# Kernel tuning notes

Hardware: AMD Instinct MI355X
Metric: run time of the kernel (lower is better)

## Reference

```python
import jax, jax.numpy as jnp
import numpy as np
import math

D = 256        # embedding_size
NHEAD = 4
HD = D // NHEAD
FF = 2048      # torch TransformerEncoderLayer default dim_feedforward
NLAYER = 3
VOCAB = 30000
OLD = 2048     # resnet50 fc in_features
BPTT = 20
EOS = 2
PAD = 0
MAXLEN = 5000


def make_pe():
    position = np.arange(MAXLEN)[:, None].astype(np.float32)
    div_term = np.exp(np.arange(0, D, 2).astype(np.float32) * (-math.log(10000.0) / D))
    pe = np.zeros((MAXLEN, D), dtype=np.float32)
    pe[:, 0::2] = np.sin(position * div_term)
    pe[:, 1::2] = np.cos(position * div_term)
    return jnp.asarray(pe)  # [maxlen, d]

PE = make_pe()


def setup_inputs() -> dict:
    key = jax.random.key(0)
    ks = jax.random.split(key, 20)
    s = 0.02
    inp = {
        'image_feats': jax.random.normal(ks[0], (64, OLD), jnp.float32),
        'target_ingrs': jax.random.randint(ks[1], (64, BPTT), 0, VOCAB),
        'emb_table': jax.random.normal(ks[2], (VOCAB, D), jnp.float32) * s,
        'W_g2e': jax.random.normal(ks[3], (OLD, D), jnp.float32) * s,
        'b_g2e': jnp.zeros((D,), jnp.float32),
        'W_out': jax.random.normal(ks[4], (D, VOCAB), jnp.float32) * s,
        'b_out': jnp.zeros((VOCAB,), jnp.float32),
    }
    # per-layer transformer params
    Wqkv, bqkv, Wo, bo, W1, b1, W2, b2, g1, be1, g2, be2 = ([] for _ in range(12))
    k = ks[5]
    for l in range(NLAYER):
        k, *sub = jax.random.split(k, 7)
        Wqkv.append(jax.random.normal(sub[0], (D, 3 * D), jnp.float32) * s)
        bqkv.append(jnp.zeros((3 * D,), jnp.float32))
        Wo.append(jax.random.normal(sub[1], (D, D), jnp.float32) * s)
        bo.append(jnp.zeros((D,), jnp.float32))
        W1.append(jax.random.normal(sub[2], (D, FF), jnp.float32) * s)
        b1.append(jnp.zeros((FF,), jnp.float32))
        W2.append(jax.random.normal(sub[3], (FF, D), jnp.float32) * s)
        b2.append(jnp.zeros((D,), jnp.float32))
        g1.append(jnp.ones((D,), jnp.float32)); be1.append(jnp.zeros((D,), jnp.float32))
        g2.append(jnp.ones((D,), jnp.float32)); be2.append(jnp.zeros((D,), jnp.float32))
    stk = lambda xs: jnp.stack(xs)
    inp.update(Wqkv=stk(Wqkv), bqkv=stk(bqkv), Wo=stk(Wo), bo=stk(bo),
               W1=stk(W1), b1=stk(b1), W2=stk(W2), b2=stk(b2),
               g1=stk(g1), be1=stk(be1), g2=stk(g2), be2=stk(be2))
    return inp


def layernorm(x, g, b):
    mu = jnp.mean(x, -1, keepdims=True)
    var = jnp.var(x, -1, keepdims=True)
    return (x - mu) * jax.lax.rsqrt(var + 1e-5) * g + b


def encoder(x, params):
    # x: [S, B, D] (seq-first like torch). Post-norm encoder, ReLU FFN, no mask.
    (Wqkv, bqkv, Wo, bo, W1, b1, W2, b2, g1, be1, g2, be2) = params
    S, B, _ = x.shape
    for l in range(NLAYER):
        qkv = x @ Wqkv[l] + bqkv[l]                  # [S,B,3D]
        q, k, v = jnp.split(qkv, 3, axis=-1)
        def heads(t):  # [S,B,D] -> [B,H,S,hd]
            return t.reshape(S, B, NHEAD, HD).transpose(1, 2, 0, 3)
        q, k, v = heads(q), heads(k), heads(v)
        att = jnp.einsum('bhqd,bhkd->bhqk', q, k) / math.sqrt(HD)
        att = jax.nn.softmax(att, axis=-1)
        o = jnp.einsum('bhqk,bhkd->bhqd', att, v)    # [B,H,S,hd]
        o = o.transpose(2, 0, 1, 3).reshape(S, B, D)
        x = layernorm(x + o @ Wo[l] + bo[l], g1[l], be1[l])
        ff = jax.nn.relu(x @ W1[l] + b1[l]) @ W2[l] + b2[l]
        x = layernorm(x + ff, g2[l], be2[l])
    return x


def mask_from_eos_after(ids):
    # mult_before=False: mask[:,idx] = all(ids[:,1:idx+1] != EOS); mask[:,0]=1
    ne = (ids != EOS)
    ne = ne.at[:, 0].set(True)
    return jnp.cumprod(ne.astype(jnp.int32), axis=1)  # [B,S]


def reference(image_feats, target_ingrs, emb_table, W_g2e, b_g2e, W_out, b_out,
              Wqkv, bqkv, Wo, bo, W1, b1, W2, b2, g1, be1, g2, be2):
    params = (Wqkv, bqkv, Wo, bo, W1, b1, W2, b2, g1, be1, g2, be2)
    B = image_feats.shape[0]
    img_embed = image_feats @ W_g2e + b_g2e          # [B,D]
    bptt = target_ingrs.shape[1]

    # embeds buffer: [bptt, B, D]; position 0 = image embed (note: original code
    # never applies pos_encoder in predict(), so neither do we)
    embeds = jnp.zeros((bptt, B, D), jnp.float32).at[0].set(img_embed)

    probs_steps = []
    words_steps = []
    # loop over decode steps (fixed-length Python loop; each step re-encodes prefix,
    # faithful to original no-KV-cache behavior)
    for i in range(bptt):
        seq = embeds[: i + 1]                        # [i+1, B, D]
        out = encoder(seq, params)[-1]               # [B, D]
        logits = out @ W_out + b_out                 # [B, V]
        sm = jax.nn.softmax(logits, axis=-1)
        widx = jnp.argmax(sm, axis=-1)               # [B]
        probs_steps.append(sm)
        words_steps.append(widx)
        if i + 1 < bptt:
            embeds = embeds.at[i + 1].set(emb_table[widx])

    decoder_out = jnp.stack(probs_steps, axis=1)     # [B, bptt, V]
    sampled_word = jnp.stack(words_steps, axis=1)    # [B, bptt]
    eos = decoder_out[:, :, EOS]
    mask = mask_from_eos_after(target_ingrs)         # [B, bptt] int
    ingr_probs = jnp.max(decoder_out * mask[:, :, None].astype(jnp.float32), axis=1)
    sampled_word = jnp.where(mask == 0, PAD, sampled_word)
    return ingr_probs, sampled_word, eos
```

## Files before the change

kernel.cpp:

```cpp
#include <hip/hip_runtime.h>
#include <math.h>

#define D 256
#define NH 4
#define HDIM 64
#define FFD 2048
#define NL 3
#define VOC 30000
#define BPTT 20
#define BATCH 64
#define NMAX (BPTT*BATCH)

__global__ void k_mask(const int* __restrict__ ids, int* __restrict__ mask) {
  int b = threadIdx.x;
  int run = 1;
  for (int j = 0; j < BPTT; ++j) {
    if (j > 0 && ids[b*BPTT + j] == 2) run = 0;
    mask[b*BPTT + j] = run;
  }
}

__global__ __launch_bounds__(256) void k_img(const float* __restrict__ feats,
                                             const float* __restrict__ Wg,
                                             const float* __restrict__ bg,
                                             float* __restrict__ embeds) {
  __shared__ float xs[2048];
  int b = blockIdx.x, tid = threadIdx.x;
  for (int j = 0; j < 8; ++j) xs[tid + j*256] = feats[b*2048 + tid + j*256];
  __syncthreads();
  float acc = 0.f;
  for (int k = 0; k < 2048; k += 4) {
    float4 xv = *(const float4*)&xs[k];
    acc += xv.x * Wg[(k+0)*D + tid];
    acc += xv.y * Wg[(k+1)*D + tid];
    acc += xv.z * Wg[(k+2)*D + tid];
    acc += xv.w * Wg[(k+3)*D + tid];
  }
  embeds[b*D + tid] = acc + bg[tid];
}

__global__ __launch_bounds__(256) void k_gemm8(
    const float* __restrict__ A, int lda,
    const float* __restrict__ W,
    const float* __restrict__ bias,
    float* __restrict__ C, long pstride,
    int klen, int M, int relu)
{
  __shared__ float As[8][256];
  const int tid  = threadIdx.x;
  const int tok0 = blockIdx.x * 8;
  const int colb = blockIdx.y * 256;
  const int z    = blockIdx.z;
  const int kbeg = z * klen;
  C += (long)z * pstride;
  const int colg = tid & 63;
  const int tokg = tid >> 6;
  const int col  = colb + colg*4;
  int colL = col;
  if (colL > M-4) colL = M-4;

  float acc[2][4] = {{0.f,0.f,0.f,0.f},{0.f,0.f,0.f,0.f}};

  for (int k0 = 0; k0 < klen; k0 += 256) {
    __syncthreads();
#pragma unroll
    for (int j = 0; j < 8; ++j)
      As[j][tid] = A[(long)(tok0 + j)*lda + kbeg + k0 + tid];
    __syncthreads();
    const float* Wp = W + (long)(kbeg + k0)*M + colL;
#pragma unroll 2
    for (int kk = 0; kk < 256; kk += 4) {
      float a[2][4], w[4][4];
      *(float4*)a[0] = *(const float4*)&As[tokg*2+0][kk];
      *(float4*)a[1] = *(const float4*)&As[tokg*2+1][kk];
      *(float4*)w[0] = *(const float4*)(Wp + (long)(kk+0)*M);
      *(float4*)w[1] = *(const float4*)(Wp + (long)(kk+1)*M);
      *(float4*)w[2] = *(const float4*)(Wp + (long)(kk+2)*M);
      *(float4*)w[3] = *(const float4*)(Wp + (long)(kk+3)*M);
#pragma unroll
      for (int j = 0; j < 2; ++j)
#pragma unroll
        for (int c = 0; c < 4; ++c)
#pragma unroll
          for (int q = 0; q < 4; ++q)
            acc[j][c] += a[j][q] * w[q][c];
    }
  }

  if (col < M) {
    float bv[4] = {0.f,0.f,0.f,0.f};
    if (bias) *(float4*)bv = *(const float4*)(bias + col);
#pragma unroll
    for (int j = 0; j < 2; ++j) {
      float v[4];
#pragma unroll
      for (int c = 0; c < 4; ++c) {
        v[c] = acc[j][c] + bv[c];
        if (relu) v[c] = fmaxf(v[c], 0.f);
      }
      *(float4*)(C + (long)(tok0 + tokg*2 + j)*M + col) = *(float4*)v;
    }
  }
}

__global__ __launch_bounds__(256) void k_resln(
    const float* __restrict__ x, const float* __restrict__ parts, int nparts, long pstride,
    const float* __restrict__ bias, const float* __restrict__ g, const float* __restrict__ be,
    float* __restrict__ out)
{
  __shared__ float red[4];
  int tok = blockIdx.x, tid = threadIdx.x;
  float v = x[(long)tok*D + tid] + bias[tid];
  for (int p = 0; p < nparts; ++p) v += parts[(long)p*pstride + (long)tok*D + tid];

  float s = v;
  for (int off = 32; off; off >>= 1) s += __shfl_down(s, off);
  if ((tid & 63) == 0) red[tid >> 6] = s;
  __syncthreads();
  float mu = (red[0]+red[1]+red[2]+red[3]) * (1.0f/D);
  __syncthreads();
  float dv = v - mu;
  float q = dv*dv;
  for (int off = 32; off; off >>= 1) q += __shfl_down(q, off);
  if ((tid & 63) == 0) red[tid >> 6] = q;
  __syncthreads();
  float var = (red[0]+red[1]+red[2]+red[3]) * (1.0f/D);
  float inv = 1.0f / sqrtf(var + 1e-5f);
  out[(long)tok*D + tid] = dv * inv * g[tid] + be[tid];
}

__global__ __launch_bounds__(64) void k_attn(const float* __restrict__ qkv,
                                             float* __restrict__ o, int S)
{
  __shared__ float qs[BPTT*HDIM], ks[BPTT*HDIM], vs[BPTT*HDIM], ps[BPTT*(BPTT+1)];
  int bh = blockIdx.x;
  int b = bh & 63, h = bh >> 6;
  int d = threadIdx.x;
  for (int s = 0; s < S; ++s) {
    long base = (long)(s*BATCH + b)*(3*D) + h*HDIM + d;
    qs[s*HDIM+d] = qkv[base];
    ks[s*HDIM+d] = qkv[base + D];
    vs[s*HDIM+d] = qkv[base + 2*D];
  }
  __syncthreads();
  for (int p = d; p < S*S; p += 64) {
    int si = p / S, ti = p - si*S;
    float acc = 0.f;
#pragma unroll 4
    for (int k = 0; k < HDIM; ++k) acc += qs[si*HDIM+k] * ks[ti*HDIM+k];
    ps[si*(BPTT+1)+ti] = acc * 0.125f;
  }
  __syncthreads();
  if (d < S) {
    float m = -1e30f;
    for (int t = 0; t < S; ++t) m = fmaxf(m, ps[d*(BPTT+1)+t]);
    float sum = 0.f;
    for (int t = 0; t < S; ++t) { float e = expf(ps[d*(BPTT+1)+t] - m); ps[d*(BPTT+1)+t] = e; sum += e; }
    float inv = 1.0f / sum;
    for (int t = 0; t < S; ++t) ps[d*(BPTT+1)+t] *= inv;
  }
  __syncthreads();
  for (int s = 0; s < S; ++s) {
    float acc = 0.f;
    for (int t = 0; t < S; ++t) acc += ps[s*(BPTT+1)+t] * vs[t*HDIM+d];
    o[(long)(s*BATCH+b)*D + h*HDIM + d] = acc;
  }
}

__global__ __launch_bounds__(256) void k_vocab(
    const float* __restrict__ logits, const int* __restrict__ mask,
    float* __restrict__ out_probs, float* __restrict__ out_words, float* __restrict__ out_eos,
    const float* __restrict__ emb, float* __restrict__ embeds, int step)
{
  __shared__ float redA[4];
  __shared__ float r_s[4];
  __shared__ float r_em[4];
  __shared__ int   r_ei[4];
  int b = blockIdx.x, tid = threadIdx.x;
  const float* lrow = logits + (long)b*VOC;

  float m = -1e30f;
  for (int c = tid; c < VOC; c += 256) m = fmaxf(m, lrow[c]);
  for (int off = 32; off; off >>= 1) m = fmaxf(m, __shfl_down(m, off));
  if ((tid & 63) == 0) redA[tid >> 6] = m;
  __syncthreads();
  float gmax = fmaxf(fmaxf(redA[0],redA[1]), fmaxf(redA[2],redA[3]));
  __syncthreads();

  float s = 0.f, em = -1.0f;
  int ei = VOC;
  for (int c = tid; c < VOC; c += 256) {
    float e = expf(lrow[c] - gmax);
    s += e;
    if (e > em) { em = e; ei = c; }
  }
  for (int off = 32; off; off >>= 1) {
    float em2 = __shfl_down(em, off);
    int   ei2 = __shfl_down(ei, off);
    if (em2 > em || (em2 == em && ei2 < ei)) { em = em2; ei = ei2; }
    s += __shfl_down(s, off);
  }
  if ((tid & 63) == 0) { r_s[tid>>6] = s; r_em[tid>>6] = em; r_ei[tid>>6] = ei; }
  __syncthreads();
  float Ssum = r_s[0]+r_s[1]+r_s[2]+r_s[3];
  em = r_em[0]; ei = r_ei[0];
  for (int w = 1; w < 4; ++w)
    if (r_em[w] > em || (r_em[w] == em && r_ei[w] < ei)) { em = r_em[w]; ei = r_ei[w]; }

  int mk = mask[b*BPTT + step];

  for (int c = tid; c < VOC; c += 256) {
    float p = expf(lrow[c] - gmax) / Ssum;
    float* op = out_probs + (long)b*VOC + c;
    if (step == 0) *op = p;
    else if (mk)   *op = fmaxf(*op, p);
    if (c == 2) out_eos[b*BPTT + step] = p;
  }
  if (tid == 0) out_words[b*BPTT + step] = mk ? (float)ei : 0.0f;
  if (step + 1 < BPTT)
    embeds[(long)((step+1)*BATCH + b)*D + tid] = emb[(long)ei*D + tid];
}

extern "C" void kernel_launch(void* const* d_in, const int* in_sizes, int n_in,
                              void* d_out, int out_size, void* d_ws, size_t ws_size,
                              hipStream_t stream) {
  const float* image_feats = (const float*)d_in[0];
  const int*   target      = (const int*)  d_in[1];
  const float* emb_table   = (const float*)d_in[2];
  const float* W_g2e       = (const float*)d_in[3];
  const float* b_g2e       = (const float*)d_in[4];
  const float* W_out       = (const float*)d_in[5];
  const float* b_out       = (const float*)d_in[6];
  const float* Wqkv        = (const float*)d_in[7];
  const float* bqkv        = (const float*)d_in[8];
  const float* Wo          = (const float*)d_in[9];
  const float* bo          = (const float*)d_in[10];
  const float* W1          = (const float*)d_in[11];
  const float* b1          = (const float*)d_in[12];
  const float* W2          = (const float*)d_in[13];
  const float* b2          = (const float*)d_in[14];
  const float* g1          = (const float*)d_in[15];
  const float* be1         = (const float*)d_in[16];
  const float* g2          = (const float*)d_in[17];
  const float* be2         = (const float*)d_in[18];

  float* out_probs = (float*)d_out;
  float* out_words = out_probs + (long)BATCH*VOC;
  float* out_eos   = out_words + BATCH*BPTT;

  char* ws = (char*)d_ws;
  float* embeds = (float*)ws;  ws += sizeof(float)*(long)NMAX*D;
  float* xbuf   = (float*)ws;  ws += sizeof(float)*(long)NMAX*D;
  float* qkvb   = (float*)ws;  ws += sizeof(float)*(long)NMAX*3*D;
  float* obuf   = (float*)ws;  ws += sizeof(float)*(long)NMAX*D;
  float* pbuf   = (float*)ws;  ws += sizeof(float)*(long)4*NMAX*D;
  float* ffb    = (float*)ws;  ws += sizeof(float)*(long)NMAX*FFD;
  float* logits = (float*)ws;  ws += sizeof(float)*(long)BATCH*VOC;
  int*   maskb  = (int*)ws;    ws += sizeof(int)*BATCH*BPTT;

  k_mask<<<1, 64, 0, stream>>>(target, maskb);
  k_img<<<64, 256, 0, stream>>>(image_feats, W_g2e, b_g2e, embeds);

  for (int i = 0; i < BPTT; ++i) {
    int N = (i+1)*BATCH;
    for (int l = 0; l < NL; ++l) {
      const float* X = (l == 0) ? embeds : xbuf;
      k_gemm8<<<dim3(N/8, 3, 1), 256, 0, stream>>>(X, D, Wqkv + (long)l*D*3*D, bqkv + (long)l*3*D,
                                                   qkvb, 0, D, 3*D, 0);
      k_attn<<<dim3(BATCH*NH), 64, 0, stream>>>(qkvb, obuf, i+1);
      k_gemm8<<<dim3(N/8, 1, 1), 256, 0, stream>>>(obuf, D, Wo + (long)l*D*D, nullptr,
                                                   pbuf, 0, D, D, 0);
      k_resln<<<dim3(N), 256, 0, stream>>>(X, pbuf, 1, 0, bo + (long)l*D, g1 + (long)l*D, be1 + (long)l*D, xbuf);
      k_gemm8<<<dim3(N/8, FFD/256, 1), 256, 0, stream>>>(xbuf, D, W1 + (long)l*D*FFD, b1 + (long)l*FFD,
                                                         ffb, 0, D, FFD, 1);
      k_gemm8<<<dim3(N/8, 1, 4), 256, 0, stream>>>(ffb, FFD, W2 + (long)l*FFD*D, nullptr,
                                                   pbuf, (long)NMAX*D, FFD/4, D, 0);
      k_resln<<<dim3(N), 256, 0, stream>>>(xbuf, pbuf, 4, (long)NMAX*D, b2 + (long)l*D, g2 + (long)l*D, be2 + (long)l*D, xbuf);
    }
    k_gemm8<<<dim3(BATCH/8, (VOC+255)/256, 1), 256, 0, stream>>>(xbuf + (long)i*BATCH*D, D, W_out, b_out,
                                                                 logits, 0, D, VOC, 0);
    k_vocab<<<dim3(BATCH), 256, 0, stream>>>(logits, maskb, out_probs, out_words, out_eos,
                                             emb_table, embeds, i);
  }
}
```

Before: 10.89 ms.

## Retile GEMM to 32x128 blocks and fuse out-projection with residual LayerNorm

Replaces the 8-token GEMM kernel with a 32-token by 128-column tiled kernel that stages A in small padded shared-memory chunks. Each weight load is now reused across four tokens per thread instead of two. Adds a fused kernel that does the attention output projection, bias, residual add and LayerNorm in one pass, removing a separate kernel launch and an intermediate buffer round trip. Larger token tiles give fewer blocks for small early steps, and the vocab GEMM now has only 2 row blocks.

```diff
diff --git a/kernel.cpp b/kernel.cpp
--- a/kernel.cpp
+++ b/kernel.cpp
@@ -39,46 +39,53 @@
   embeds[b*D + tid] = acc + bg[tid];
 }
 
-__global__ __launch_bounds__(256) void k_gemm8(
+__global__ __launch_bounds__(256) void k_gemm32(
     const float* __restrict__ A, int lda,
     const float* __restrict__ W,
     const float* __restrict__ bias,
     float* __restrict__ C, long pstride,
     int klen, int M, int relu)
 {
-  __shared__ float As[8][256];
+  __shared__ float As[32][36];
   const int tid  = threadIdx.x;
-  const int tok0 = blockIdx.x * 8;
-  const int colb = blockIdx.y * 256;
+  const int tok0 = blockIdx.x * 32;
+  const int colb = blockIdx.y * 128;
   const int z    = blockIdx.z;
   const int kbeg = z * klen;
   C += (long)z * pstride;
-  const int colg = tid & 63;
-  const int tokg = tid >> 6;
+
+  const int colg = tid & 31;
+  const int tokg = tid >> 5;
   const int col  = colb + colg*4;
-  int colL = col;
-  if (colL > M-4) colL = M-4;
-
-  float acc[2][4] = {{0.f,0.f,0.f,0.f},{0.f,0.f,0.f,0.f}};
-
-  for (int k0 = 0; k0 < klen; k0 += 256) {
+  int colL = col; if (colL > M-4) colL = M-4;
+
+  const int sr = tid >> 3;
+  const int sc = (tid & 7) * 4;
+
+  float acc[4][4];
+#pragma unroll
+  for (int j = 0; j < 4; ++j)
+#pragma unroll
+    for (int c = 0; c < 4; ++c) acc[j][c] = 0.f;
+
+  for (int k0 = 0; k0 < klen; k0 += 32) {
     __syncthreads();
-#pragma unroll
-    for (int j = 0; j < 8; ++j)
-      As[j][tid] = A[(long)(tok0 + j)*lda + kbeg + k0 + tid];
+    *(float4*)&As[sr][sc] = *(const float4*)&A[(long)(tok0 + sr)*lda + kbeg + k0 + sc];
     __syncthreads();
     const float* Wp = W + (long)(kbeg + k0)*M + colL;
-#pragma unroll 2
-    for (int kk = 0; kk < 256; kk += 4) {
-      float a[2][4], w[4][4];
-      *(float4*)a[0] = *(const float4*)&As[tokg*2+0][kk];
-      *(float4*)a[1] = *(const float4*)&As[tokg*2+1][kk];
+#pragma unroll
+    for (int kk = 0; kk < 32; kk += 4) {
+      float w[4][4], a[4][4];
       *(float4*)w[0] = *(const float4*)(Wp + (long)(kk+0)*M);
       *(float4*)w[1] = *(const float4*)(Wp + (long)(kk+1)*M);
       *(float4*)w[2] = *(const float4*)(Wp + (long)(kk+2)*M);
       *(float4*)w[3] = *(const float4*)(Wp + (long)(kk+3)*M);
-#pragma unroll
-      for (int j = 0; j < 2; ++j)
+      *(float4*)a[0] = *(const float4*)&As[tokg*4+0][kk];
+      *(float4*)a[1] = *(const float4*)&As[tokg*4+1][kk];
+      *(float4*)a[2] = *(const float4*)&As[tokg*4+2][kk];
+      *(float4*)a[3] = *(const float4*)&As[tokg*4+3][kk];
+#pragma unroll
+      for (int j = 0; j < 4; ++j)
 #pragma unroll
         for (int c = 0; c < 4; ++c)
 #pragma unroll
@@ -91,15 +98,97 @@
     float bv[4] = {0.f,0.f,0.f,0.f};
     if (bias) *(float4*)bv = *(const float4*)(bias + col);
 #pragma unroll
-    for (int j = 0; j < 2; ++j) {
+    for (int j = 0; j < 4; ++j) {
       float v[4];
 #pragma unroll
       for (int c = 0; c < 4; ++c) {
         v[c] = acc[j][c] + bv[c];
         if (relu) v[c] = fmaxf(v[c], 0.f);
       }
-      *(float4*)(C + (long)(tok0 + tokg*2 + j)*M + col) = *(float4*)v;
+      *(float4*)(C + (long)(tok0 + tokg*4 + j)*M + col) = *(float4*)v;
     }
+  }
+}
+
+__global__ __launch_bounds__(256) void k_projln(
+    const float* __restrict__ Aop,
+    const float* __restrict__ W,
+    const float* __restrict__ X,
+    const float* __restrict__ bias,
+    const float* __restrict__ g, const float* __restrict__ be,
+    float* __restrict__ out)
+{
+  __shared__ float As[16][68];
+  const int tid  = threadIdx.x;
+  const int tok0 = blockIdx.x * 16;
+  const int colg = tid & 63;
+  const int tokg = tid >> 6;
+  const int col  = colg * 4;
+
+  const int sr = tid >> 4;
+  const int sc = (tid & 15) * 4;
+
+  float acc[4][4];
+#pragma unroll
+  for (int j = 0; j < 4; ++j)
+#pragma unroll
+    for (int c = 0; c < 4; ++c) acc[j][c] = 0.f;
+
+  for (int k0 = 0; k0 < 256; k0 += 64) {
+    __syncthreads();
+    *(float4*)&As[sr][sc] = *(const float4*)&Aop[(long)(tok0 + sr)*D + k0 + sc];
+    __syncthreads();
+    const float* Wp = W + (long)k0*D + col;
+#pragma unroll
+    for (int kk = 0; kk < 64; kk += 4) {
+      float w[4][4], a[4][4];
+      *(float4*)w[0] = *(const float4*)(Wp + (long)(kk+0)*D);
+      *(float4*)w[1] = *(const float4*)(Wp + (long)(kk+1)*D);
+      *(float4*)w[2] = *(const float4*)(Wp + (long)(kk+2)*D);
+      *(float4*)w[3] = *(const float4*)(Wp + (long)(kk+3)*D);
+      *(float4*)a[0] = *(const float4*)&As[tokg*4+0][kk];
+      *(float4*)a[1] = *(const float4*)&As[tokg*4+1][kk];
+      *(float4*)a[2] = *(const float4*)&As[tokg*4+2][kk];
+      *(float4*)a[3] = *(const float4*)&As[tokg*4+3][kk];
+#pragma unroll
+      for (int j = 0; j < 4; ++j)
+#pragma unroll
+        for (int c = 0; c < 4; ++c)
+#pragma unroll
+          for (int q = 0; q < 4; ++q)
+            acc[j][c] += a[j][q] * w[q][c];
+    }
+  }
+
+  float bv[4], gv[4], bev[4];
+  *(float4*)bv  = *(const float4*)(bias + col);
+  *(float4*)gv  = *(const float4*)(g + col);
+  *(float4*)bev = *(const float4*)(be + col);
+
+#pragma unroll
+  for (int j = 0; j < 4; ++j) {
+    const int tok = tok0 + tokg*4 + j;
+    float v[4];
+    float4 xv = *(const float4*)(X + (long)tok*D + col);
+    v[0] = acc[j][0] + bv[0] + xv.x;
+    v[1] = acc[j][1] + bv[1] + xv.y;
+    v[2] = acc[j][2] + bv[2] + xv.z;
+    v[3] = acc[j][3] + bv[3] + xv.w;
+    float s = v[0]+v[1]+v[2]+v[3];
+#pragma unroll
+    for (int off = 1; off < 64; off <<= 1) s += __shfl_xor(s, off);
+    float mu = s * (1.0f/D);
+    float q0=v[0]-mu, q1=v[1]-mu, q2=v[2]-mu, q3=v[3]-mu;
+    float q = q0*q0+q1*q1+q2*q2+q3*q3;
+#pragma unroll
+    for (int off = 1; off < 64; off <<= 1) q += __shfl_xor(q, off);
+    float inv = 1.0f / sqrtf(q * (1.0f/D) + 1e-5f);
+    float o[4];
+    o[0] = q0*inv*gv[0] + bev[0];
+    o[1] = q1*inv*gv[1] + bev[1];
+    o[2] = q2*inv*gv[2] + bev[2];
+    o[3] = q3*inv*gv[3] + bev[3];
+    *(float4*)(out + (long)tok*D + col) = *(float4*)o;
   }
 }
 
@@ -265,20 +354,19 @@
     int N = (i+1)*BATCH;
     for (int l = 0; l < NL; ++l) {
       const float* X = (l == 0) ? embeds : xbuf;
-      k_gemm8<<<dim3(N/8, 3, 1), 256, 0, stream>>>(X, D, Wqkv + (long)l*D*3*D, bqkv + (long)l*3*D,
-                                                   qkvb, 0, D, 3*D, 0);
+      k_gemm32<<<dim3(N/32, 6, 1), 256, 0, stream>>>(X, D, Wqkv + (long)l*D*3*D, bqkv + (long)l*3*D,
+                                                     qkvb, 0, D, 3*D, 0);
       k_attn<<<dim3(BATCH*NH), 64, 0, stream>>>(qkvb, obuf, i+1);
-      k_gemm8<<<dim3(N/8, 1, 1), 256, 0, stream>>>(obuf, D, Wo + (long)l*D*D, nullptr,
-                                                   pbuf, 0, D, D, 0);
-      k_resln<<<dim3(N), 256, 0, stream>>>(X, pbuf, 1, 0, bo + (long)l*D, g1 + (long)l*D, be1 + (long)l*D, xbuf);
-      k_gemm8<<<dim3(N/8, FFD/256, 1), 256, 0, stream>>>(xbuf, D, W1 + (long)l*D*FFD, b1 + (long)l*FFD,
-                                                         ffb, 0, D, FFD, 1);
-      k_gemm8<<<dim3(N/8, 1, 4), 256, 0, stream>>>(ffb, FFD, W2 + (long)l*FFD*D, nullptr,
-                                                   pbuf, (long)NMAX*D, FFD/4, D, 0);
+      k_projln<<<dim3(N/16), 256, 0, stream>>>(obuf, Wo + (long)l*D*D, X, bo + (long)l*D,
+                                               g1 + (long)l*D, be1 + (long)l*D, xbuf);
+      k_gemm32<<<dim3(N/32, FFD/128, 1), 256, 0, stream>>>(xbuf, D, W1 + (long)l*D*FFD, b1 + (long)l*FFD,
+                                                           ffb, 0, D, FFD, 1);
+      k_gemm32<<<dim3(N/32, 2, 4), 256, 0, stream>>>(ffb, FFD, W2 + (long)l*FFD*D, nullptr,
+                                                     pbuf, (long)NMAX*D, FFD/4, D, 0);
       k_resln<<<dim3(N), 256, 0, stream>>>(xbuf, pbuf, 4, (long)NMAX*D, b2 + (long)l*D, g2 + (long)l*D, be2 + (long)l*D, xbuf);
     }
-    k_gemm8<<<dim3(BATCH/8, (VOC+255)/256, 1), 256, 0, stream>>>(xbuf + (long)i*BATCH*D, D, W_out, b_out,
-                                                                 logits, 0, D, VOC, 0);
+    k_gemm32<<<dim3(BATCH/32, (VOC+127)/128, 1), 256, 0, stream>>>(xbuf + (long)i*BATCH*D, D, W_out, b_out,
+                                                                   logits, 0, D, VOC, 0);
     k_vocab<<<dim3(BATCH), 256, 0, stream>>>(logits, maskb, out_probs, out_words, out_eos,
                                              emb_table, embeds, i);
   }
```

Result: slower. 18.37 ms (+68.7%).

## Replace per-stage launches with one persistent cooperative megakernel using grid syncs

Applied to the files above, without the earlier changes.

Replaces the roughly 400 small kernel launches with a single cooperative persistent kernel. Each stage is a grid-stride loop over tiles, separated by grid.sync. The out-projection GEMM is fused with residual-add and LayerNorm, and attention now uses 256 threads per unit with a padded K buffer. This aims to remove launch overhead and idle gaps between the many tiny dependent kernels, at the cost of grid-wide barriers and a fixed grid size (at most 512 blocks). A multi-launch fallback runs if the cooperative launch fails.

```diff
diff --git a/kernel.cpp b/kernel.cpp
--- a/kernel.cpp
+++ b/kernel.cpp
@@ -1,5 +1,8 @@
 #include <hip/hip_runtime.h>
+#include <hip/hip_cooperative_groups.h>
 #include <math.h>
+
+namespace cg = cooperative_groups;
 
 #define D 256
 #define NH 4
@@ -11,21 +14,264 @@
 #define BATCH 64
 #define NMAX (BPTT*BATCH)
 
-__global__ void k_mask(const int* __restrict__ ids, int* __restrict__ mask) {
-  int b = threadIdx.x;
-  int run = 1;
-  for (int j = 0; j < BPTT; ++j) {
-    if (j > 0 && ids[b*BPTT + j] == 2) run = 0;
-    mask[b*BPTT + j] = run;
-  }
-}
-
-__global__ __launch_bounds__(256) void k_img(const float* __restrict__ feats,
-                                             const float* __restrict__ Wg,
-                                             const float* __restrict__ bg,
-                                             float* __restrict__ embeds) {
-  __shared__ float xs[2048];
-  int b = blockIdx.x, tid = threadIdx.x;
+struct Args {
+  const float* image_feats; const int* target; const float* emb_table;
+  const float* W_g2e; const float* b_g2e; const float* W_out; const float* b_out;
+  const float* Wqkv; const float* bqkv; const float* Wo; const float* bo;
+  const float* W1; const float* b1; const float* W2; const float* b2;
+  const float* g1; const float* be1; const float* g2; const float* be2;
+  float* out_probs; float* out_words; float* out_eos;
+  float* embeds; float* xbuf; float* qkvb; float* obuf; float* pbuf; float* ffb; float* logits;
+  int* maskb;
+};
+
+
+__device__ __forceinline__ void gemm_tile(
+    float* As, const float* __restrict__ A, int lda,
+    const float* __restrict__ W, const float* __restrict__ bias,
+    float* __restrict__ C, int M, int klen, int kbeg, int relu,
+    int tok0, int colb, int tid)
+{
+  const int colg = tid & 63;
+  const int tokg = tid >> 6;
+  const int col  = colb + colg*4;
+  int colL = col; if (colL > M-4) colL = M-4;
+
+  float acc[2][4] = {{0.f,0.f,0.f,0.f},{0.f,0.f,0.f,0.f}};
+
+  for (int k0 = 0; k0 < klen; k0 += 256) {
+    __syncthreads();
+#pragma unroll
+    for (int j = 0; j < 8; ++j)
+      As[j*256 + tid] = A[(long)(tok0 + j)*lda + kbeg + k0 + tid];
+    __syncthreads();
+    const float* Wp = W + (long)(kbeg + k0)*M + colL;
+#pragma unroll 2
+    for (int kk = 0; kk < 256; kk += 4) {
+      float a0[4], a1[4], w[4][4];
+      *(float4*)a0   = *(const float4*)&As[(tokg*2+0)*256 + kk];
+      *(float4*)a1   = *(const float4*)&As[(tokg*2+1)*256 + kk];
+      *(float4*)w[0] = *(const float4*)(Wp + (long)(kk+0)*M);
+      *(float4*)w[1] = *(const float4*)(Wp + (long)(kk+1)*M);
+      *(float4*)w[2] = *(const float4*)(Wp + (long)(kk+2)*M);
+      *(float4*)w[3] = *(const float4*)(Wp + (long)(kk+3)*M);
+#pragma unroll
+      for (int c = 0; c < 4; ++c)
+#pragma unroll
+        for (int q = 0; q < 4; ++q) {
+          acc[0][c] += a0[q] * w[q][c];
+          acc[1][c] += a1[q] * w[q][c];
+        }
+    }
+  }
+
+  if (col < M) {
+    float bv[4] = {0.f,0.f,0.f,0.f};
+    if (bias) *(float4*)bv = *(const float4*)(bias + col);
+#pragma unroll
+    for (int j = 0; j < 2; ++j) {
+      float v[4];
+#pragma unroll
+      for (int c = 0; c < 4; ++c) {
+        v[c] = acc[j][c] + bv[c];
+        if (relu) v[c] = fmaxf(v[c], 0.f);
+      }
+      *(float4*)(C + (long)(tok0 + tokg*2 + j)*M + col) = *(float4*)v;
+    }
+  }
+}
+
+__device__ __forceinline__ void projln_tile(
+    float* As, const float* __restrict__ Aop, const float* __restrict__ W,
+    const float* __restrict__ X, const float* __restrict__ bias,
+    const float* __restrict__ g, const float* __restrict__ be,
+    float* __restrict__ out, int tok0, int tid)
+{
+  const int colg = tid & 63;
+  const int tokg = tid >> 6;
+  const int col  = colg*4;
+
+  float acc[2][4] = {{0.f,0.f,0.f,0.f},{0.f,0.f,0.f,0.f}};
+
+  __syncthreads();
+#pragma unroll
+  for (int j = 0; j < 8; ++j)
+    As[j*256 + tid] = Aop[(long)(tok0 + j)*D + tid];
+  __syncthreads();
+  const float* Wp = W + col;
+#pragma unroll 2
+  for (int kk = 0; kk < 256; kk += 4) {
+    float a0[4], a1[4], w[4][4];
+    *(float4*)a0   = *(const float4*)&As[(tokg*2+0)*256 + kk];
+    *(float4*)a1   = *(const float4*)&As[(tokg*2+1)*256 + kk];
+    *(float4*)w[0] = *(const float4*)(Wp + (long)(kk+0)*D);
+    *(float4*)w[1] = *(const float4*)(Wp + (long)(kk+1)*D);
+    *(float4*)w[2] = *(const float4*)(Wp + (long)(kk+2)*D);
+    *(float4*)w[3] = *(const float4*)(Wp + (long)(kk+3)*D);
+#pragma unroll
+    for (int c = 0; c < 4; ++c)
+#pragma unroll
+      for (int q = 0; q < 4; ++q) {
+        acc[0][c] += a0[q] * w[q][c];
+        acc[1][c] += a1[q] * w[q][c];
+      }
+  }
+
+  float bv[4], gv[4], bev[4];
+  *(float4*)bv  = *(const float4*)(bias + col);
+  *(float4*)gv  = *(const float4*)(g + col);
+  *(float4*)bev = *(const float4*)(be + col);
+
+#pragma unroll
+  for (int j = 0; j < 2; ++j) {
+    const int tok = tok0 + tokg*2 + j;
+    float v[4];
+    float4 xv = *(const float4*)(X + (long)tok*D + col);
+    v[0] = acc[j][0] + bv[0] + xv.x;
+    v[1] = acc[j][1] + bv[1] + xv.y;
+    v[2] = acc[j][2] + bv[2] + xv.z;
+    v[3] = acc[j][3] + bv[3] + xv.w;
+    float s = v[0]+v[1]+v[2]+v[3];
+#pragma unroll
+    for (int off = 1; off < 64; off <<= 1) s += __shfl_xor(s, off);
+    float mu = s * (1.0f/D);
+    float q0=v[0]-mu, q1=v[1]-mu, q2=v[2]-mu, q3=v[3]-mu;
+    float q = q0*q0+q1*q1+q2*q2+q3*q3;
+#pragma unroll
+    for (int off = 1; off < 64; off <<= 1) q += __shfl_xor(q, off);
+    float inv = 1.0f / sqrtf(q * (1.0f/D) + 1e-5f);
+    float o[4];
+    o[0] = q0*inv*gv[0] + bev[0];
+    o[1] = q1*inv*gv[1] + bev[1];
+    o[2] = q2*inv*gv[2] + bev[2];
+    o[3] = q3*inv*gv[3] + bev[3];
+    *(float4*)(out + (long)tok*D + col) = *(float4*)o;
+  }
+}
+
+__device__ __forceinline__ void resln_token(
+    const float* __restrict__ x, const float* __restrict__ parts, long pstride,
+    const float* __restrict__ bias, const float* __restrict__ g,
+    const float* __restrict__ be, float* __restrict__ out,
+    int tok, int tid, float* red)
+{
+  float v = x[(long)tok*D + tid] + bias[tid];
+#pragma unroll
+  for (int p = 0; p < 4; ++p) v += parts[(long)p*pstride + (long)tok*D + tid];
+  float s = v;
+  for (int off = 32; off; off >>= 1) s += __shfl_down(s, off);
+  if ((tid & 63) == 0) red[tid >> 6] = s;
+  __syncthreads();
+  float mu = (red[0]+red[1]+red[2]+red[3]) * (1.0f/D);
+  __syncthreads();
+  float dv = v - mu;
+  float q = dv*dv;
+  for (int off = 32; off; off >>= 1) q += __shfl_down(q, off);
+  if ((tid & 63) == 0) red[tid >> 6] = q;
+  __syncthreads();
+  float var = (red[0]+red[1]+red[2]+red[3]) * (1.0f/D);
+  out[(long)tok*D + tid] = dv * (1.0f/sqrtf(var + 1e-5f)) * g[tid] + be[tid];
+  __syncthreads();
+}
+
+__device__ __forceinline__ void attn_unit(
+    float* sm, const float* __restrict__ qkv, float* __restrict__ o,
+    int S, int unit, int tid)
+{
+  float* qs = sm;
+  float* ks = sm + 1280;
+  float* vs = sm + 2640;
+  float* ps = sm + 3920;
+  const int b = unit & 63, h = unit >> 6;
+  __syncthreads();
+  for (int idx = tid; idx < S*HDIM; idx += 256) {
+    int s = idx >> 6, dd = idx & 63;
+    long base = (long)(s*BATCH + b)*(3*D) + h*HDIM + dd;
+    qs[idx]        = qkv[base];
+    ks[s*68 + dd]  = qkv[base + D];
+    vs[idx]        = qkv[base + 2*D];
+  }
+  __syncthreads();
+  for (int p = tid; p < S*S; p += 256) {
+    int si = p / S, ti = p - si*S;
+    float acc = 0.f;
+#pragma unroll 8
+    for (int k = 0; k < HDIM; ++k) acc += qs[si*HDIM + k] * ks[ti*68 + k];
+    ps[si*(BPTT+1) + ti] = acc * 0.125f;
+  }
+  __syncthreads();
+  if (tid < S) {
+    float m = -1e30f;
+    for (int t = 0; t < S; ++t) m = fmaxf(m, ps[tid*(BPTT+1)+t]);
+    float sum = 0.f;
+    for (int t = 0; t < S; ++t) { float e = expf(ps[tid*(BPTT+1)+t] - m); ps[tid*(BPTT+1)+t] = e; sum += e; }
+    float inv = 1.0f / sum;
+    for (int t = 0; t < S; ++t) ps[tid*(BPTT+1)+t] *= inv;
+  }
+  __syncthreads();
+  for (int idx = tid; idx < S*HDIM; idx += 256) {
+    int s = idx >> 6, dd = idx & 63;
+    float acc = 0.f;
+    for (int t = 0; t < S; ++t) acc += ps[s*(BPTT+1)+t] * vs[t*HDIM + dd];
+    o[(long)(s*BATCH + b)*D + h*HDIM + dd] = acc;
+  }
+}
+
+__device__ __forceinline__ void vocab_unit(
+    float* redf, int* redi,
+    const float* __restrict__ logits, const int* __restrict__ mask,
+    float* __restrict__ out_probs, float* __restrict__ out_words, float* __restrict__ out_eos,
+    const float* __restrict__ emb, float* __restrict__ embeds, int step, int b, int tid)
+{
+  const float* lrow = logits + (long)b*VOC;
+  __syncthreads();
+  float m = -1e30f;
+  for (int c = tid; c < VOC; c += 256) m = fmaxf(m, lrow[c]);
+  for (int off = 32; off; off >>= 1) m = fmaxf(m, __shfl_down(m, off));
+  if ((tid & 63) == 0) redf[tid >> 6] = m;
+  __syncthreads();
+  float gmax = fmaxf(fmaxf(redf[0],redf[1]), fmaxf(redf[2],redf[3]));
+  __syncthreads();
+
+  float s = 0.f, em = -1.0f;
+  int ei = VOC;
+  for (int c = tid; c < VOC; c += 256) {
+    float e = expf(lrow[c] - gmax);
+    s += e;
+    if (e > em) { em = e; ei = c; }
+  }
+  for (int off = 32; off; off >>= 1) {
+    float em2 = __shfl_down(em, off);
+    int   ei2 = __shfl_down(ei, off);
+    if (em2 > em || (em2 == em && ei2 < ei)) { em = em2; ei = ei2; }
+    s += __shfl_down(s, off);
+  }
+  if ((tid & 63) == 0) { redf[4+(tid>>6)] = s; redf[8+(tid>>6)] = em; redi[tid>>6] = ei; }
+  __syncthreads();
+  float Ssum = redf[4]+redf[5]+redf[6]+redf[7];
+  em = redf[8]; ei = redi[0];
+  for (int w = 1; w < 4; ++w)
+    if (redf[8+w] > em || (redf[8+w] == em && redi[w] < ei)) { em = redf[8+w]; ei = redi[w]; }
+
+  int mk = mask[b*BPTT + step];
+  for (int c = tid; c < VOC; c += 256) {
+    float p = expf(lrow[c] - gmax) / Ssum;
+    float* op = out_probs + (long)b*VOC + c;
+    if (step == 0) *op = p;
+    else if (mk)   *op = fmaxf(*op, p);
+    if (c == 2) out_eos[b*BPTT + step] = p;
+  }
+  if (tid == 0) out_words[b*BPTT + step] = mk ? (float)ei : 0.0f;
+  if (step + 1 < BPTT)
+    embeds[(long)((step+1)*BATCH + b)*D + tid] = emb[(long)ei*D + tid];
+  __syncthreads();
+}
+
+__device__ __forceinline__ void img_unit(
+    float* xs, const float* __restrict__ feats, const float* __restrict__ Wg,
+    const float* __restrict__ bg, float* __restrict__ embeds, int b, int tid)
+{
+  __syncthreads();
   for (int j = 0; j < 8; ++j) xs[tid + j*256] = feats[b*2048 + tid + j*256];
   __syncthreads();
   float acc = 0.f;
@@ -39,247 +285,182 @@
   embeds[b*D + tid] = acc + bg[tid];
 }
 
-__global__ __launch_bounds__(256) void k_gemm8(
-    const float* __restrict__ A, int lda,
-    const float* __restrict__ W,
-    const float* __restrict__ bias,
-    float* __restrict__ C, long pstride,
-    int klen, int M, int relu)
-{
-  __shared__ float As[8][256];
-  const int tid  = threadIdx.x;
-  const int tok0 = blockIdx.x * 8;
-  const int colb = blockIdx.y * 256;
-  const int z    = blockIdx.z;
-  const int kbeg = z * klen;
-  C += (long)z * pstride;
-  const int colg = tid & 63;
-  const int tokg = tid >> 6;
-  const int col  = colb + colg*4;
-  int colL = col;
-  if (colL > M-4) colL = M-4;
-
-  float acc[2][4] = {{0.f,0.f,0.f,0.f},{0.f,0.f,0.f,0.f}};
-
-  for (int k0 = 0; k0 < klen; k0 += 256) {
-    __syncthreads();
-#pragma unroll
-    for (int j = 0; j < 8; ++j)
-      As[j][tid] = A[(long)(tok0 + j)*lda + kbeg + k0 + tid];
-    __syncthreads();
-    const float* Wp = W + (long)(kbeg + k0)*M + colL;
-#pragma unroll 2
-    for (int kk = 0; kk < 256; kk += 4) {
-      float a[2][4], w[4][4];
-      *(float4*)a[0] = *(const float4*)&As[tokg*2+0][kk];
-      *(float4*)a[1] = *(const float4*)&As[tokg*2+1][kk];
-      *(float4*)w[0] = *(const float4*)(Wp + (long)(kk+0)*M);
-      *(float4*)w[1] = *(const float4*)(Wp + (long)(kk+1)*M);
-      *(float4*)w[2] = *(const float4*)(Wp + (long)(kk+2)*M);
-      *(float4*)w[3] = *(const float4*)(Wp + (long)(kk+3)*M);
-#pragma unroll
-      for (int j = 0; j < 2; ++j)
-#pragma unroll
-        for (int c = 0; c < 4; ++c)
-#pragma unroll
-          for (int q = 0; q < 4; ++q)
-            acc[j][c] += a[j][q] * w[q][c];
-    }
-  }
-
-  if (col < M) {
-    float bv[4] = {0.f,0.f,0.f,0.f};
-    if (bias) *(float4*)bv = *(const float4*)(bias + col);
-#pragma unroll
-    for (int j = 0; j < 2; ++j) {
-      float v[4];
-#pragma unroll
-      for (int c = 0; c < 4; ++c) {
-        v[c] = acc[j][c] + bv[c];
-        if (relu) v[c] = fmaxf(v[c], 0.f);
-      }
-      *(float4*)(C + (long)(tok0 + tokg*2 + j)*M + col) = *(float4*)v;
-    }
-  }
-}
-
-__global__ __launch_bounds__(256) void k_resln(
-    const float* __restrict__ x, const float* __restrict__ parts, int nparts, long pstride,
-    const float* __restrict__ bias, const float* __restrict__ g, const float* __restrict__ be,
-    float* __restrict__ out)
-{
+__global__ __launch_bounds__(256, 2) void mega(Args a) {
+  __shared__ float sm[4352];
+  __shared__ float redf[16];
+  __shared__ int   redi[4];
+  cg::grid_group grid = cg::this_grid();
+  const int tid = threadIdx.x;
+  const int nb  = gridDim.x;
+
+  if (blockIdx.x == 0 && tid < 64) {
+    int b = tid, run = 1;
+    for (int j = 0; j < BPTT; ++j) {
+      if (j > 0 && a.target[b*BPTT + j] == 2) run = 0;
+      a.maskb[b*BPTT + j] = run;
+    }
+  }
+  for (int t = blockIdx.x; t < BATCH; t += nb)
+    img_unit(sm, a.image_feats, a.W_g2e, a.b_g2e, a.embeds, t, tid);
+  grid.sync();
+
+  for (int i = 0; i < BPTT; ++i) {
+    const int S = i + 1, N = S * BATCH, ntt = N / 8;
+    for (int l = 0; l < NL; ++l) {
+      const float* X = (l == 0) ? a.embeds : a.xbuf;
+      for (int t = blockIdx.x; t < ntt*3; t += nb) {
+        int tt = t % ntt, cb = t / ntt;
+        gemm_tile(sm, X, D, a.Wqkv + (long)l*D*3*D, a.bqkv + (long)l*3*D,
+                  a.qkvb, 3*D, 256, 0, 0, tt*8, cb*256, tid);
+      }
+      grid.sync();
+      for (int t = blockIdx.x; t < BATCH*NH; t += nb)
+        attn_unit(sm, a.qkvb, a.obuf, S, t, tid);
+      grid.sync();
+      for (int t = blockIdx.x; t < ntt; t += nb)
+        projln_tile(sm, a.obuf, a.Wo + (long)l*D*D, X, a.bo + (long)l*D,
+                    a.g1 + (long)l*D, a.be1 + (long)l*D, a.xbuf, t*8, tid);
+      grid.sync();
+      for (int t = blockIdx.x; t < ntt*8; t += nb) {
+        int tt = t % ntt, cb = t / ntt;
+        gemm_tile(sm, a.xbuf, D, a.W1 + (long)l*D*FFD, a.b1 + (long)l*FFD,
+                  a.ffb, FFD, 256, 0, 1, tt*8, cb*256, tid);
+      }
+      grid.sync();
+      for (int t = blockIdx.x; t < ntt*4; t += nb) {
+        int tt = t % ntt, z = t / ntt;
+        gemm_tile(sm, a.ffb, FFD, a.W2 + (long)l*FFD*D, nullptr,
+                  a.pbuf + (long)z*NMAX*D, D, 512, z*512, 0, tt*8, 0, tid);
+      }
+      grid.sync();
+      for (int t = blockIdx.x; t < N; t += nb)
+        resln_token(a.xbuf, a.pbuf, (long)NMAX*D, a.b2 + (long)l*D,
+                    a.g2 + (long)l*D, a.be2 + (long)l*D, a.xbuf, t, tid, redf);
+      grid.sync();
+    }
+    const float* Xl = a.xbuf + (long)i*BATCH*D;
+    for (int t = blockIdx.x; t < 8*118; t += nb) {
+      int tt = t % 8, cb = t / 8;
+      gemm_tile(sm, Xl, D, a.W_out, a.b_out, a.logits, VOC, 256, 0, 0, tt*8, cb*256, tid);
+    }
+    grid.sync();
+    for (int t = blockIdx.x; t < BATCH; t += nb)
+      vocab_unit(redf, redi, a.logits, a.maskb, a.out_probs, a.out_words, a.out_eos,
+                 a.emb_table, a.embeds, i, t, tid);
+    grid.sync();
+  }
+}
+
+__global__ void k_mask(const int* __restrict__ ids, int* __restrict__ mask) {
+  int b = threadIdx.x, run = 1;
+  for (int j = 0; j < BPTT; ++j) {
+    if (j > 0 && ids[b*BPTT + j] == 2) run = 0;
+    mask[b*BPTT + j] = run;
+  }
+}
+__global__ __launch_bounds__(256) void k_img(const float* f, const float* Wg, const float* bg, float* e) {
+  __shared__ float xs[2048];
+  img_unit(xs, f, Wg, bg, e, blockIdx.x, threadIdx.x);
+}
+__global__ __launch_bounds__(256) void k_gemm(const float* A, int lda, const float* W, const float* bias,
+                                              float* C, long pstride, int klen, int M, int relu) {
+  __shared__ float As[2048];
+  gemm_tile(As, A, lda, W, bias, C + (long)blockIdx.z*pstride, M, klen, blockIdx.z*klen, relu,
+            blockIdx.x*8, blockIdx.y*256, threadIdx.x);
+}
+__global__ __launch_bounds__(256) void k_projln(const float* Aop, const float* W, const float* X,
+                                                const float* bias, const float* g, const float* be, float* out) {
+  __shared__ float As[2048];
+  projln_tile(As, Aop, W, X, bias, g, be, out, blockIdx.x*8, threadIdx.x);
+}
+__global__ __launch_bounds__(256) void k_resln(const float* x, const float* parts, long pstride,
+                                               const float* bias, const float* g, const float* be, float* out) {
   __shared__ float red[4];
-  int tok = blockIdx.x, tid = threadIdx.x;
-  float v = x[(long)tok*D + tid] + bias[tid];
-  for (int p = 0; p < nparts; ++p) v += parts[(long)p*pstride + (long)tok*D + tid];
-
-  float s = v;
-  for (int off = 32; off; off >>= 1) s += __shfl_down(s, off);
-  if ((tid & 63) == 0) red[tid >> 6] = s;
-  __syncthreads();
-  float mu = (red[0]+red[1]+red[2]+red[3]) * (1.0f/D);
-  __syncthreads();
-  float dv = v - mu;
-  float q = dv*dv;
-  for (int off = 32; off; off >>= 1) q += __shfl_down(q, off);
-  if ((tid & 63) == 0) red[tid >> 6] = q;
-  __syncthreads();
-  float var = (red[0]+red[1]+red[2]+red[3]) * (1.0f/D);
-  float inv = 1.0f / sqrtf(var + 1e-5f);
-  out[(long)tok*D + tid] = dv * inv * g[tid] + be[tid];
-}
-
-__global__ __launch_bounds__(64) void k_attn(const float* __restrict__ qkv,
-                                             float* __restrict__ o, int S)
-{
-  __shared__ float qs[BPTT*HDIM], ks[BPTT*HDIM], vs[BPTT*HDIM], ps[BPTT*(BPTT+1)];
-  int bh = blockIdx.x;
-  int b = bh & 63, h = bh >> 6;
-  int d = threadIdx.x;
-  for (int s = 0; s < S; ++s) {
-    long base = (long)(s*BATCH + b)*(3*D) + h*HDIM + d;
-    qs[s*HDIM+d] = qkv[base];
-    ks[s*HDIM+d] = qkv[base + D];
-    vs[s*HDIM+d] = qkv[base + 2*D];
-  }
-  __syncthreads();
-  for (int p = d; p < S*S; p += 64) {
-    int si = p / S, ti = p - si*S;
-    float acc = 0.f;
-#pragma unroll 4
-    for (int k = 0; k < HDIM; ++k) acc += qs[si*HDIM+k] * ks[ti*HDIM+k];
-    ps[si*(BPTT+1)+ti] = acc * 0.125f;
-  }
-  __syncthreads();
-  if (d < S) {
-    float m = -1e30f;
-    for (int t = 0; t < S; ++t) m = fmaxf(m, ps[d*(BPTT+1)+t]);
-    float sum = 0.f;
-    for (int t = 0; t < S; ++t) { float e = expf(ps[d*(BPTT+1)+t] - m); ps[d*(BPTT+1)+t] = e; sum += e; }
-    float inv = 1.0f / sum;
-    for (int t = 0; t < S; ++t) ps[d*(BPTT+1)+t] *= inv;
-  }
-  __syncthreads();
-  for (int s = 0; s < S; ++s) {
-    float acc = 0.f;
-    for (int t = 0; t < S; ++t) acc += ps[s*(BPTT+1)+t] * vs[t*HDIM+d];
-    o[(long)(s*BATCH+b)*D + h*HDIM + d] = acc;
-  }
-}
-
-__global__ __launch_bounds__(256) void k_vocab(
-    const float* __restrict__ logits, const int* __restrict__ mask,
-    float* __restrict__ out_probs, float* __restrict__ out_words, float* __restrict__ out_eos,
-    const float* __restrict__ emb, float* __restrict__ embeds, int step)
-{
-  __shared__ float redA[4];
-  __shared__ float r_s[4];
-  __shared__ float r_em[4];
-  __shared__ int   r_ei[4];
-  int b = blockIdx.x, tid = threadIdx.x;
-  const float* lrow = logits + (long)b*VOC;
-
-  float m = -1e30f;
-  for (int c = tid; c < VOC; c += 256) m = fmaxf(m, lrow[c]);
-  for (int off = 32; off; off >>= 1) m = fmaxf(m, __shfl_down(m, off));
-  if ((tid & 63) == 0) redA[tid >> 6] = m;
-  __syncthreads();
-  float gmax = fmaxf(fmaxf(redA[0],redA[1]), fmaxf(redA[2],redA[3]));
-  __syncthreads();
-
-  float s = 0.f, em = -1.0f;
-  int ei = VOC;
-  for (int c = tid; c < VOC; c += 256) {
-    float e = expf(lrow[c] - gmax);
-    s += e;
-    if (e > em) { em = e; ei = c; }
-  }
-  for (int off = 32; off; off >>= 1) {
-    float em2 = __shfl_down(em, off);
-    int   ei2 = __shfl_down(ei, off);
-    if (em2 > em || (em2 == em && ei2 < ei)) { em = em2; ei = ei2; }
-    s += __shfl_down(s, off);
-  }
-  if ((tid & 63) == 0) { r_s[tid>>6] = s; r_em[tid>>6] = em; r_ei[tid>>6] = ei; }
-  __syncthreads();
-  float Ssum = r_s[0]+r_s[1]+r_s[2]+r_s[3];
-  em = r_em[0]; ei = r_ei[0];
-  for (int w = 1; w < 4; ++w)
-    if (r_em[w] > em || (r_em[w] == em && r_ei[w] < ei)) { em = r_em[w]; ei = r_ei[w]; }
-
-  int mk = mask[b*BPTT + step];
-
-  for (int c = tid; c < VOC; c += 256) {
-    float p = expf(lrow[c] - gmax) / Ssum;
-    float* op = out_probs + (long)b*VOC + c;
-    if (step == 0) *op = p;
-    else if (mk)   *op = fmaxf(*op, p);
-    if (c == 2) out_eos[b*BPTT + step] = p;
-  }
-  if (tid == 0) out_words[b*BPTT + step] = mk ? (float)ei : 0.0f;
-  if (step + 1 < BPTT)
-    embeds[(long)((step+1)*BATCH + b)*D + tid] = emb[(long)ei*D + tid];
+  resln_token(x, parts, pstride, bias, g, be, out, blockIdx.x, threadIdx.x, red);
+}
+__global__ __launch_bounds__(256) void k_attn(const float* qkv, float* o, int S) {
+  __shared__ float sm[4352];
+  attn_unit(sm, qkv, o, S, blockIdx.x, threadIdx.x);
+}
+__global__ __launch_bounds__(256) void k_vocab(const float* logits, const int* mask,
+    float* out_probs, float* out_words, float* out_eos,
+    const float* emb, float* embeds, int step) {
+  __shared__ float redf[16];
+  __shared__ int   redi[4];
+  vocab_unit(redf, redi, logits, mask, out_probs, out_words, out_eos, emb, embeds, step,
+             blockIdx.x, threadIdx.x);
 }
 
 extern "C" void kernel_launch(void* const* d_in, const int* in_sizes, int n_in,
                               void* d_out, int out_size, void* d_ws, size_t ws_size,
                               hipStream_t stream) {
-  const float* image_feats = (const float*)d_in[0];
-  const int*   target      = (const int*)  d_in[1];
-  const float* emb_table   = (const float*)d_in[2];
-  const float* W_g2e       = (const float*)d_in[3];
-  const float* b_g2e       = (const float*)d_in[4];
-  const float* W_out       = (const float*)d_in[5];
-  const float* b_out       = (const float*)d_in[6];
-  const float* Wqkv        = (const float*)d_in[7];
-  const float* bqkv        = (const float*)d_in[8];
-  const float* Wo          = (const float*)d_in[9];
-  const float* bo          = (const float*)d_in[10];
-  const float* W1          = (const float*)d_in[11];
-  const float* b1          = (const float*)d_in[12];
-  const float* W2          = (const float*)d_in[13];
-  const float* b2          = (const float*)d_in[14];
-  const float* g1          = (const float*)d_in[15];
-  const float* be1         = (const float*)d_in[16];
-  const float* g2          = (const float*)d_in[17];
-  const float* be2         = (const float*)d_in[18];
-
-  float* out_probs = (float*)d_out;
-  float* out_words = out_probs + (long)BATCH*VOC;
-  float* out_eos   = out_words + BATCH*BPTT;
+  Args a;
+  a.image_feats = (const float*)d_in[0];
+  a.target      = (const int*)  d_in[1];
+  a.emb_table   = (const float*)d_in[2];
+  a.W_g2e       = (const float*)d_in[3];
+  a.b_g2e       = (const float*)d_in[4];
+  a.W_out       = (const float*)d_in[5];
+  a.b_out       = (const float*)d_in[6];
+  a.Wqkv        = (const float*)d_in[7];
+  a.bqkv        = (const float*)d_in[8];
+  a.Wo          = (const float*)d_in[9];
+  a.bo          = (const float*)d_in[10];
+  a.W1          = (const float*)d_in[11];
+  a.b1          = (const float*)d_in[12];
+  a.W2          = (const float*)d_in[13];
+  a.b2          = (const float*)d_in[14];
+  a.g1          = (const float*)d_in[15];
+  a.be1         = (const float*)d_in[16];
+  a.g2          = (const float*)d_in[17];
+  a.be2         = (const float*)d_in[18];
+
+  a.out_probs = (float*)d_out;
+  a.out_words = a.out_probs + (long)BATCH*VOC;
+  a.out_eos   = a.out_words + BATCH*BPTT;
 
   char* ws = (char*)d_ws;
-  float* embeds = (float*)ws;  ws += sizeof(float)*(long)NMAX*D;
-  float* xbuf   = (float*)ws;  ws += sizeof(float)*(long)NMAX*D;
-  float* qkvb   = (float*)ws;  ws += sizeof(float)*(long)NMAX*3*D;
-  float* obuf   = (float*)ws;  ws += sizeof(float)*(long)NMAX*D;
-  float* pbuf   = (float*)ws;  ws += sizeof(float)*(long)4*NMAX*D;
-  float* ffb    = (float*)ws;  ws += sizeof(float)*(long)NMAX*FFD;
-  float* logits = (float*)ws;  ws += sizeof(float)*(long)BATCH*VOC;
-  int*   maskb  = (int*)ws;    ws += sizeof(int)*BATCH*BPTT;
-
-  k_mask<<<1, 64, 0, stream>>>(target, maskb);
-  k_img<<<64, 256, 0, stream>>>(image_feats, W_g2e, b_g2e, embeds);
-
-  for (int i = 0; i < BPTT; ++i) {
-    int N = (i+1)*BATCH;
-    for (int l = 0; l < NL; ++l) {
-      const float* X = (l == 0) ? embeds : xbuf;
-      k_gemm8<<<dim3(N/8, 3, 1), 256, 0, stream>>>(X, D, Wqkv + (long)l*D*3*D, bqkv + (long)l*3*D,
-                                                   qkvb, 0, D, 3*D, 0);
-      k_attn<<<dim3(BATCH*NH), 64, 0, stream>>>(qkvb, obuf, i+1);
-      k_gemm8<<<dim3(N/8, 1, 1), 256, 0, stream>>>(obuf, D, Wo + (long)l*D*D, nullptr,
-                                                   pbuf, 0, D, D, 0);
-      k_resln<<<dim3(N), 256, 0, stream>>>(X, pbuf, 1, 0, bo + (long)l*D, g1 + (long)l*D, be1 + (long)l*D, xbuf);
-      k_gemm8<<<dim3(N/8, FFD/256, 1), 256, 0, stream>>>(xbuf, D, W1 + (long)l*D*FFD, b1 + (long)l*FFD,
-                                                         ffb, 0, D, FFD, 1);
-      k_gemm8<<<dim3(N/8, 1, 4), 256, 0, stream>>>(ffb, FFD, W2 + (long)l*FFD*D, nullptr,
-                                                   pbuf, (long)NMAX*D, FFD/4, D, 0);
-      k_resln<<<dim3(N), 256, 0, stream>>>(xbuf, pbuf, 4, (long)NMAX*D, b2 + (long)l*D, g2 + (long)l*D, be2 + (long)l*D, xbuf);
-    }
-    k_gemm8<<<dim3(BATCH/8, (VOC+255)/256, 1), 256, 0, stream>>>(xbuf + (long)i*BATCH*D, D, W_out, b_out,
-                                                                 logits, 0, D, VOC, 0);
-    k_vocab<<<dim3(BATCH), 256, 0, stream>>>(logits, maskb, out_probs, out_words, out_eos,
-                                             emb_table, embeds, i);
-  }
-}
+  a.embeds = (float*)ws;  ws += sizeof(float)*(long)NMAX*D;
+  a.xbuf   = (float*)ws;  ws += sizeof(float)*(long)NMAX*D;
+  a.qkvb   = (float*)ws;  ws += sizeof(float)*(long)NMAX*3*D;
+  a.obuf   = (float*)ws;  ws += sizeof(float)*(long)NMAX*D;
+  a.pbuf   = (float*)ws;  ws += sizeof(float)*(long)4*NMAX*D;
+  a.ffb    = (float*)ws;  ws += sizeof(float)*(long)NMAX*FFD;
+  a.logits = (float*)ws;  ws += sizeof(float)*(long)BATCH*VOC;
+  a.maskb  = (int*)ws;    ws += sizeof(int)*BATCH*BPTT;
+
+  int occ = 0;
+  hipError_t oe = hipOccupancyMaxActiveBlocksPerMultiprocessor(&occ, (const void*)mega, 256, 0);
+  if (oe != hipSuccess || occ < 1) occ = 1;
+  int grid = occ * 256;
+  if (grid > 512) grid = 512;
+
+  void* params[1] = { (void*)&a };
+  hipError_t e = hipLaunchCooperativeKernel((const void*)mega, dim3(grid), dim3(256), params, 0, stream);
+
+  if (e != hipSuccess) {
+    k_mask<<<1, 64, 0, stream>>>(a.target, a.maskb);
+    k_img<<<BATCH, 256, 0, stream>>>(a.image_feats, a.W_g2e, a.b_g2e, a.embeds);
+    for (int i = 0; i < BPTT; ++i) {
+      int S = i+1, N = S*BATCH, ntt = N/8;
+      for (int l = 0; l < NL; ++l) {
+        const float* X = (l == 0) ? a.embeds : a.xbuf;
+        k_gemm<<<dim3(ntt,3,1), 256, 0, stream>>>(X, D, a.Wqkv + (long)l*D*3*D, a.bqkv + (long)l*3*D,
+                                                  a.qkvb, 0, 256, 3*D, 0);
+        k_attn<<<dim3(BATCH*NH), 256, 0, stream>>>(a.qkvb, a.obuf, S);
+        k_projln<<<dim3(ntt), 256, 0, stream>>>(a.obuf, a.Wo + (long)l*D*D, X, a.bo + (long)l*D,
+                                                a.g1 + (long)l*D, a.be1 + (long)l*D, a.xbuf);
+        k_gemm<<<dim3(ntt,8,1), 256, 0, stream>>>(a.xbuf, D, a.W1 + (long)l*D*FFD, a.b1 + (long)l*FFD,
+                                                  a.ffb, 0, 256, FFD, 1);
+        k_gemm<<<dim3(ntt,1,4), 256, 0, stream>>>(a.ffb, FFD, a.W2 + (long)l*FFD*D, nullptr,
+                                                  a.pbuf, (long)NMAX*D, 512, D, 0);
+        k_resln<<<dim3(N), 256, 0, stream>>>(a.xbuf, a.pbuf, (long)NMAX*D, a.b2 + (long)l*D,
+                                             a.g2 + (long)l*D, a.be2 + (long)l*D, a.xbuf);
+      }
+      k_gemm<<<dim3(8,118,1), 256, 0, stream>>>(a.xbuf + (long)i*BATCH*D, D, a.W_out, a.b_out,
+                                                a.logits, 0, 256, VOC, 0);
+      k_vocab<<<dim3(BATCH), 256, 0, stream>>>(a.logits, a.maskb, a.out_probs, a.out_words, a.out_eos,
+                                               a.emb_table, a.embeds, i);
+    }
+  }
+}
```

New measurement: 21.87 ms. +100.9%, slower.
